# Performance work log

Hardware: AMD Instinct MI355X
Metric: run time of the kernel (lower is better)

## Reference

```python
import jax, jax.numpy as jnp
import numpy as np

EMBED = 1024
B, S = 4, 2048


def setup_inputs() -> dict:
    key = jax.random.key(0)
    ks = jax.random.split(key, 10)
    scale = 1.0 / np.sqrt(EMBED)
    return {
        "query": jax.random.normal(ks[0], (B, S, EMBED), jnp.float32),
        "key": jax.random.normal(ks[1], (B, S, EMBED), jnp.float32),
        "value": jax.random.normal(ks[2], (B, S, EMBED), jnp.float32),
        "attn_mask": jnp.zeros((B, S, S), jnp.float32),
        "Wq": jax.random.normal(ks[3], (EMBED, EMBED), jnp.float32) * scale,
        "bq": jnp.zeros((EMBED,), jnp.float32),
        "Wk": jax.random.normal(ks[4], (EMBED, EMBED), jnp.float32) * scale,
        "bk": jnp.zeros((EMBED,), jnp.float32),
        "Wv": jax.random.normal(ks[5], (EMBED, EMBED), jnp.float32) * scale,
        "bv": jnp.zeros((EMBED,), jnp.float32),
    }


def reference(query, key, value, attn_mask, Wq, bq, Wk, bk, Wv, bv):
    # Linear projections (torch Linear: x @ W.T + b)
    q = jnp.einsum("bse,fe->bsf", query, Wq) + bq
    k = jnp.einsum("bse,fe->bsf", key, Wk) + bk
    v = jnp.einsum("bse,fe->bsf", value, Wv) + bv
    # Scaled dot-product attention; NOTE: scale is sqrt(embed_size) (full dim),
    # matching the original module exactly (num_heads is unused there).
    inv_scale = 1.0 / jnp.sqrt(jnp.asarray(q.shape[-1], q.dtype))
    qk = jnp.einsum("bqe,bke->bqk", q, k) * inv_scale + attn_mask
    attn = jax.nn.softmax(qk, axis=-1)
    # dropout_p = 0.0 (eval-mode identity)
    return jnp.einsum("bqk,bke->bqe", attn, v)
```

## Files before the change

kernel.cpp:

```cpp
#include <hip/hip_runtime.h>
#include <stdint.h>


typedef __attribute__((ext_vector_type(8))) short s8v;
typedef __attribute__((ext_vector_type(4))) float f32x4;
typedef __attribute__((ext_vector_type(4))) unsigned u32x4;

__device__ __forceinline__ unsigned short f2b(float f) {
  union { float f; unsigned u; } c; c.f = f;
  unsigned r = c.u + 0x7fffu + ((c.u >> 16) & 1u);
  return (unsigned short)(r >> 16);
}

__device__ __forceinline__ void gload_lds16(const void* gsrc, void* ldst) {
  __builtin_amdgcn_global_load_lds(
      (__attribute__((address_space(1))) unsigned int*)(uintptr_t)gsrc,
      (__attribute__((address_space(3))) unsigned int*)(unsigned)(uintptr_t)ldst,
      16, 0, 0);
}

template <int N> __device__ __forceinline__ void waitvm() {
  if constexpr (N == 4)      asm volatile("s_waitcnt vmcnt(4)" ::: "memory");
  else if constexpr (N == 3) asm volatile("s_waitcnt vmcnt(3)" ::: "memory");
  else                       asm volatile("s_waitcnt vmcnt(0)" ::: "memory");
}

struct JobF {
  const float* A; const float* B; unsigned short* C; const float* bias;
  long sAb, sBb, sCb;
  int lda, ldb, ldc, tilesN, tilesMN, bmode;
};

__global__ __launch_bounds__(512, 2) void gemmF(JobF j0, JobF j1, JobF j2,
                                                int b0, int b1) {
  constexpr int ASLOT = 256 * 64;
  constexpr int SLOT = ASLOT + 128 * 64;
  constexpr int NT = 32;
  __shared__ __align__(16) char lds[4 * SLOT];

  const int nwg = gridDim.x;
  const int hw = blockIdx.x;
  int g = (hw & 7) * (nwg >> 3) + (hw >> 3);
  const JobF J = (g < b0) ? j0 : (g < b1) ? j1 : j2;
  g -= (g < b0) ? 0 : (g < b1) ? b0 : b1;

  const int batch = g / J.tilesMN;
  const int tt = g - batch * J.tilesMN;
  const int tm = tt / J.tilesN, tn = tt - tm * J.tilesN;
  const int brow = tm << 8, bcol = tn << 7;

  const int tid = threadIdx.x, lane = tid & 63, w = tid >> 6;
  const int wm = w >> 2, wn = w & 3;
  const int fr = lane & 15, fq = lane >> 4;

  const float* Ab = J.A + (long)batch * J.sAb;
  const float* Bb = J.B + (long)batch * J.sBb;

  const float* gsrcF[3];
  int ldsdst[3];
#pragma unroll
  for (int i = 0; i < 3; i++) {
    const int c = w + i * 8;
    const bool isA = (c < 16);
    const int cc = isA ? c : c - 16;
    const int roff = cc * 1024 + lane * 16;
    const int L = roff ^ (((roff >> 7) & 7) << 4);
    const int row = L >> 6, elem = (L & 63) >> 1;
    gsrcF[i] = (isA ? (Ab + (long)(brow + row) * J.lda)
                    : (Bb + (long)(bcol + row) * J.ldb)) + elem;
    ldsdst[i] = (isA ? 0 : ASLOT) + cc * 1024 + lane * 16;
  }

  int offA[8], offB[2];
#pragma unroll
  for (int mi = 0; mi < 8; mi++) {
    const int oa = (wm * 128 + mi * 16 + fr) * 64 + fq * 16;
    offA[mi] = oa ^ (((oa >> 7) & 7) << 4);
  }
#pragma unroll
  for (int ni = 0; ni < 2; ni++) {
    const int ob = (wn * 32 + ni * 16 + fr) * 64 + fq * 16;
    offB[ni] = ASLOT + (ob ^ (((ob >> 7) & 7) << 4));
  }

  f32x4 acc[8][2];
#pragma unroll
  for (int mi = 0; mi < 8; mi++)
#pragma unroll
    for (int ni = 0; ni < 2; ni++) acc[mi][ni] = (f32x4){0.f, 0.f, 0.f, 0.f};

  f32x4 eLo[3], eHi[3], oLo[3], oHi[3];

#define ISSUE(kt, LO, HI) { \
  _Pragma("unroll") \
  for (int i_ = 0; i_ < 3; i_++) { \
    const float* p_ = gsrcF[i_] + (long)(kt) * 32; \
    LO[i_] = *(const f32x4*)p_; HI[i_] = *(const f32x4*)(p_ + 4); } }

#define CVTWRITE(kt, LO, HI) { \
  char* const sb_ = lds + ((kt) & 3) * SLOT; \
  _Pragma("unroll") \
  for (int i_ = 0; i_ < 3; i_++) { \
    unsigned o0_, o1_, o2_, o3_; \
    asm("v_cvt_pk_bf16_f32 %0, %1, %2" : "=v"(o0_) : "v"(LO[i_][0]), "v"(LO[i_][1])); \
    asm("v_cvt_pk_bf16_f32 %0, %1, %2" : "=v"(o1_) : "v"(LO[i_][2]), "v"(LO[i_][3])); \
    asm("v_cvt_pk_bf16_f32 %0, %1, %2" : "=v"(o2_) : "v"(HI[i_][0]), "v"(HI[i_][1])); \
    asm("v_cvt_pk_bf16_f32 %0, %1, %2" : "=v"(o3_) : "v"(HI[i_][2]), "v"(HI[i_][3])); \
    *(u32x4*)(sb_ + ldsdst[i_]) = (u32x4){o0_, o1_, o2_, o3_}; } }

#define MFMA_BODY(t) { \
  const char* sb_ = lds + ((t) & 3) * SLOT; \
  s8v bf_[2], af_[4]; \
  _Pragma("unroll") \
  for (int ni_ = 0; ni_ < 2; ni_++) bf_[ni_] = *(const s8v*)(sb_ + offB[ni_]); \
  _Pragma("unroll") \
  for (int mi_ = 0; mi_ < 4; mi_++) af_[mi_] = *(const s8v*)(sb_ + offA[mi_]); \
  __builtin_amdgcn_s_setprio(1); \
  _Pragma("unroll") \
  for (int mi_ = 0; mi_ < 4; mi_++) \
    _Pragma("unroll") \
    for (int ni_ = 0; ni_ < 2; ni_++) \
      acc[mi_][ni_] = __builtin_amdgcn_mfma_f32_16x16x32_bf16( \
          af_[mi_], bf_[ni_], acc[mi_][ni_], 0, 0, 0); \
  __builtin_amdgcn_s_setprio(0); \
  _Pragma("unroll") \
  for (int mi_ = 0; mi_ < 4; mi_++) af_[mi_] = *(const s8v*)(sb_ + offA[4 + mi_]); \
  __builtin_amdgcn_s_setprio(1); \
  _Pragma("unroll") \
  for (int mi_ = 0; mi_ < 4; mi_++) \
    _Pragma("unroll") \
    for (int ni_ = 0; ni_ < 2; ni_++) \
      acc[4 + mi_][ni_] = __builtin_amdgcn_mfma_f32_16x16x32_bf16( \
          af_[mi_], bf_[ni_], acc[4 + mi_][ni_], 0, 0, 0); \
  __builtin_amdgcn_s_setprio(0); }

#define ENDBAR() { \
  asm volatile("s_waitcnt lgkmcnt(0)" ::: "memory"); \
  __builtin_amdgcn_s_barrier(); }

  ISSUE(0, eLo, eHi);
  ISSUE(1, oLo, oHi);
  CVTWRITE(0, eLo, eHi);
  ENDBAR();
  ISSUE(2, eLo, eHi);

  for (int t = 0; t < NT; t += 2) {
    MFMA_BODY(t);
    if (t + 1 < NT) {
      CVTWRITE(t + 1, oLo, oHi);
      if (t + 3 < NT) ISSUE(t + 3, oLo, oHi);
      ENDBAR();
      MFMA_BODY(t + 1);
      if (t + 2 < NT) {
        CVTWRITE(t + 2, eLo, eHi);
        if (t + 4 < NT) ISSUE(t + 4, eLo, eHi);
        ENDBAR();
      }
    }
  }

  const long cB = (long)batch * J.sCb;
#pragma unroll
  for (int mi = 0; mi < 8; mi++) {
    const int rbase = brow + wm * 128 + mi * 16 + fq * 4;
#pragma unroll
    for (int ni = 0; ni < 2; ni++) {
      const int col = bcol + wn * 32 + ni * 16 + fr;
      const float bc = (J.bmode == 1) ? J.bias[col] : 0.f;
#pragma unroll
      for (int r = 0; r < 4; r++) {
        const int row = rbase + r;
        float v = acc[mi][ni][r] + ((J.bmode == 2) ? J.bias[row] : bc);
        J.C[cB + (long)row * J.ldc + col] = f2b(v);
      }
    }
  }
#undef ISSUE
#undef CVTWRITE
#undef MFMA_BODY
#undef ENDBAR
}

struct Job {
  const unsigned short* A; const unsigned short* B; void* C;
  const float* bias; const float* mask; float* sRow;
  long sAb, sBb, sCb, sMb;
  int lda, ldb, ldc, ldM;
  int K, tilesN, tilesMN;
  float scale; int bmode;
};

template <int NFRAG, int MODE>
__global__ __launch_bounds__(512, 2) void gemmJ(Job j0, Job j1, Job j2,
                                                int b0, int b1) {
  constexpr int BN = NFRAG * 64;
  constexpr int ASLOT = 256 * 64;
  constexpr int BSLOT = BN * 64;
  constexpr int SLOT = ASLOT + BSLOT;
  constexpr int CH = SLOT / 1024;
  constexpr int GPW = CH / 8;
  static_assert(4 * SLOT <= 160 * 1024, "LDS budget");
  __shared__ __align__(16) char lds[4 * SLOT];

  const int nwg = gridDim.x;
  const int hw = blockIdx.x;
  int g = (hw & 7) * (nwg >> 3) + (hw >> 3);
  const Job J = (g < b0) ? j0 : (g < b1) ? j1 : j2;
  g -= (g < b0) ? 0 : (g < b1) ? b0 : b1;

  const int batch = g / J.tilesMN;
  const int tt = g - batch * J.tilesMN;
  const int tm = tt / J.tilesN, tn = tt - tm * J.tilesN;
  const int brow = tm << 8, bcol = tn * BN;

  const int tid = threadIdx.x;
  const int lane = tid & 63, w = tid >> 6;
  const int wm = w >> 2, wn = w & 3;
  const int fr = lane & 15, fq = lane >> 4;

  const unsigned short* Ab = J.A + (long)batch * J.sAb;
  const unsigned short* Bb = J.B + (long)batch * J.sBb;

  const unsigned short* gsrc[GPW];
  int ldsdst[GPW];
#pragma unroll
  for (int i = 0; i < GPW; i++) {
    const int c = w + i * 8;
    const bool isA = (c < 16);
    const int cc = isA ? c : c - 16;
    const int roff = cc * 1024 + lane * 16;
    const int L = roff ^ (((roff >> 7) & 7) << 4);
    const int row = L >> 6, colb = L & 63;
    gsrc[i] = (isA ? (Ab + (long)(brow + row) * J.lda)
                   : (Bb + (long)(bcol + row) * J.ldb)) + (colb >> 1);
    ldsdst[i] = (isA ? 0 : ASLOT) + cc * 1024;
  }

  int offA[8], offB[NFRAG];
#pragma unroll
  for (int mi = 0; mi < 8; mi++) {
    const int oa = (wm * 128 + mi * 16 + fr) * 64 + fq * 16;
    offA[mi] = oa ^ (((oa >> 7) & 7) << 4);
  }
#pragma unroll
  for (int ni = 0; ni < NFRAG; ni++) {
    const int ob = (wn * (NFRAG * 16) + ni * 16 + fr) * 64 + fq * 16;
    offB[ni] = ASLOT + (ob ^ (((ob >> 7) & 7) << 4));
  }

  f32x4 acc[8][NFRAG];
#pragma unroll
  for (int mi = 0; mi < 8; mi++)
#pragma unroll
    for (int ni = 0; ni < NFRAG; ni++) acc[mi][ni] = (f32x4){0.f, 0.f, 0.f, 0.f};

  const int NT = J.K >> 5;

#define STAGE(kt) { \
  char* const sb_ = lds + ((kt) & 3) * SLOT; \
  _Pragma("unroll") \
  for (int i_ = 0; i_ < GPW; i_++) \
    gload_lds16(gsrc[i_] + (long)(kt) * 32, sb_ + ldsdst[i_]); }

  STAGE(0);
  STAGE(1);
  waitvm<GPW>();
  __builtin_amdgcn_s_barrier();

  for (int t = 0; t < NT; ++t) {
    const char* sb = lds + (t & 3) * SLOT;
    if (t + 2 < NT) STAGE(t + 2);

    s8v bf[NFRAG], af[4];
#pragma unroll
    for (int ni = 0; ni < NFRAG; ni++) bf[ni] = *(const s8v*)(sb + offB[ni]);
#pragma unroll
    for (int mi = 0; mi < 4; mi++) af[mi] = *(const s8v*)(sb + offA[mi]);
    __builtin_amdgcn_s_setprio(1);
#pragma unroll
    for (int mi = 0; mi < 4; mi++)
#pragma unroll
      for (int ni = 0; ni < NFRAG; ni++)
        acc[mi][ni] = __builtin_amdgcn_mfma_f32_16x16x32_bf16(
            af[mi], bf[ni], acc[mi][ni], 0, 0, 0);
    __builtin_amdgcn_s_setprio(0);
#pragma unroll
    for (int mi = 0; mi < 4; mi++) af[mi] = *(const s8v*)(sb + offA[4 + mi]);
    __builtin_amdgcn_s_setprio(1);
#pragma unroll
    for (int mi = 0; mi < 4; mi++)
#pragma unroll
      for (int ni = 0; ni < NFRAG; ni++)
        acc[4 + mi][ni] = __builtin_amdgcn_mfma_f32_16x16x32_bf16(
            af[mi], bf[ni], acc[4 + mi][ni], 0, 0, 0);
    __builtin_amdgcn_s_setprio(0);

    if (t + 1 < NT) {
      if (t + 2 < NT) waitvm<GPW>();
      else            waitvm<0>();
      __builtin_amdgcn_s_barrier();
    }
  }

  unsigned short* Cb = (unsigned short*)J.C;
  float* Cf = (float*)J.C;
  const long cB = (long)batch * J.sCb;
  const float* maskB = (MODE == 1) ? (J.mask + (long)batch * J.sMb) : nullptr;
  float* sB = (J.sRow != nullptr) ? (J.sRow + batch * 2048) : nullptr;

#pragma unroll
  for (int mi = 0; mi < 8; mi++) {
    const int rbase = brow + wm * 128 + mi * 16 + fq * 4;

    if constexpr (MODE == 1) {
      float rs[4] = {0.f, 0.f, 0.f, 0.f};
#pragma unroll
      for (int ni = 0; ni < NFRAG; ni++) {
        const int col = bcol + wn * (NFRAG * 16) + ni * 16 + fr;
#pragma unroll
        for (int r = 0; r < 4; r++) {
          const int row = rbase + r;
          float v = acc[mi][ni][r] * J.scale + maskB[(long)row * J.ldM + col];
          v = __expf(v);
          Cb[cB + (long)row * J.ldc + col] = f2b(v);
          rs[r] += v;
        }
      }
#pragma unroll
      for (int off = 1; off < 16; off <<= 1) {
#pragma unroll
        for (int r = 0; r < 4; r++) rs[r] += __shfl_xor(rs[r], off, 64);
      }
      if (fr == 0) {
#pragma unroll
        for (int r = 0; r < 4; r++) atomicAdd(&sB[rbase + r], rs[r]);
      }
    } else {
      float inv[4];
#pragma unroll
      for (int r = 0; r < 4; r++) inv[r] = 1.0f / sB[rbase + r];
#pragma unroll
      for (int ni = 0; ni < NFRAG; ni++) {
        const int col = bcol + wn * (NFRAG * 16) + ni * 16 + fr;
#pragma unroll
        for (int r = 0; r < 4; r++) {
          const int row = rbase + r;
          Cf[cB + (long)row * J.ldc + col] = acc[mi][ni][r] * inv[r];
        }
      }
    }
  }
#undef STAGE
}

__global__ __launch_bounds__(256) void zeroS(float* sz) {
  sz[blockIdx.x * 256 + threadIdx.x] = 0.f;
}

extern "C" void kernel_launch(void* const* d_in, const int* in_sizes, int n_in,
                              void* d_out, int out_size, void* d_ws, size_t ws_size,
                              hipStream_t stream) {
  const float* q    = (const float*)d_in[0];
  const float* k    = (const float*)d_in[1];
  const float* v    = (const float*)d_in[2];
  const float* mask = (const float*)d_in[3];
  const float* Wq   = (const float*)d_in[4];
  const float* bq   = (const float*)d_in[5];
  const float* Wk   = (const float*)d_in[6];
  const float* bk   = (const float*)d_in[7];
  const float* Wv   = (const float*)d_in[8];
  const float* bv   = (const float*)d_in[9];
  float* out = (float*)d_out;

  const size_t MB = 1ull << 20;
  if (ws_size < 134 * MB) return;
  char* ws = (char*)d_ws;
  unsigned short* qb  = (unsigned short*)(ws + 0 * MB);
  unsigned short* kb  = (unsigned short*)(ws + 16 * MB);
  unsigned short* vT  = (unsigned short*)(ws + 32 * MB);
  float*          sRw = (float*)(ws + 48 * MB);
  unsigned short* Sb  = (unsigned short*)(ws + 80 * MB);

  zeroS<<<32, 256, 0, stream>>>(sRw);

  JobF fq = { q, Wq, qb, bq, 0, 0, 0, 1024, 1024, 1024, 8, 256, 1 };
  JobF fk = { k, Wk, kb, bk, 0, 0, 0, 1024, 1024, 1024, 8, 256, 1 };
  JobF fv = { Wv, v, vT, bv, 0, 2048L * 1024, 1024L * 2048,
              1024, 1024, 2048, 16, 64, 2 };
  gemmF<<<768, 512, 0, stream>>>(fq, fk, fv, 256, 512);

  Job js = { qb, kb, (void*)Sb, nullptr, mask, sRw,
             2048L * 1024, 2048L * 1024, 2048L * 2048, 2048L * 2048,
             1024, 1024, 2048, 2048, 1024, 8, 64, 0.03125f, 0 };
  gemmJ<4, 1><<<256, 512, 0, stream>>>(js, js, js, 256, 256);

  Job jp = { Sb, vT, (void*)out, nullptr, nullptr, sRw,
             2048L * 2048, 1024L * 2048, 2048L * 1024, 0,
             2048, 2048, 1024, 0, 2048, 8, 64, 1.0f, 0 };
  gemmJ<2, 2><<<256, 512, 0, stream>>>(jp, jp, jp, 256, 256);
}
```

Measured before the change: 221.6 us.

## Double K-tile depth in fp32-input projection GEMM with triple-buffered LDS

```diff
diff --git a/kernel.cpp b/kernel.cpp
--- a/kernel.cpp
+++ b/kernel.cpp
@@ -31,12 +31,12 @@
   int lda, ldb, ldc, tilesN, tilesMN, bmode;
 };
 
-__global__ __launch_bounds__(512, 2) void gemmF(JobF j0, JobF j1, JobF j2,
+__global__ __launch_bounds__(512, 1) void gemmF(JobF j0, JobF j1, JobF j2,
                                                 int b0, int b1) {
-  constexpr int ASLOT = 256 * 64;
-  constexpr int SLOT = ASLOT + 128 * 64;
-  constexpr int NT = 32;
-  __shared__ __align__(16) char lds[4 * SLOT];
+  constexpr int ASLOT = 256 * 128;
+  constexpr int SLOT = ASLOT + 128 * 128;
+  constexpr int NT = 16;
+  __shared__ __align__(16) char lds[3 * SLOT];
 
   const int nwg = gridDim.x;
   const int hw = blockIdx.x;
@@ -56,16 +56,16 @@
   const float* Ab = J.A + (long)batch * J.sAb;
   const float* Bb = J.B + (long)batch * J.sBb;
 
-  const float* gsrcF[3];
-  int ldsdst[3];
-#pragma unroll
-  for (int i = 0; i < 3; i++) {
+  const float* gsrcF[6];
+  int ldsdst[6];
+#pragma unroll
+  for (int i = 0; i < 6; i++) {
     const int c = w + i * 8;
-    const bool isA = (c < 16);
-    const int cc = isA ? c : c - 16;
+    const bool isA = (c < 32);
+    const int cc = isA ? c : c - 32;
     const int roff = cc * 1024 + lane * 16;
     const int L = roff ^ (((roff >> 7) & 7) << 4);
-    const int row = L >> 6, elem = (L & 63) >> 1;
+    const int row = L >> 7, elem = (L & 127) >> 1;
     gsrcF[i] = (isA ? (Ab + (long)(brow + row) * J.lda)
                     : (Bb + (long)(bcol + row) * J.ldb)) + elem;
     ldsdst[i] = (isA ? 0 : ASLOT) + cc * 1024 + lane * 16;
@@ -74,13 +74,13 @@
   int offA[8], offB[2];
 #pragma unroll
   for (int mi = 0; mi < 8; mi++) {
-    const int oa = (wm * 128 + mi * 16 + fr) * 64 + fq * 16;
-    offA[mi] = oa ^ (((oa >> 7) & 7) << 4);
+    const int rA = wm * 128 + mi * 16 + fr;
+    offA[mi] = rA * 128 + ((fq * 16) ^ ((rA & 7) << 4));
   }
 #pragma unroll
   for (int ni = 0; ni < 2; ni++) {
-    const int ob = (wn * 32 + ni * 16 + fr) * 64 + fq * 16;
-    offB[ni] = ASLOT + (ob ^ (((ob >> 7) & 7) << 4));
+    const int rB = wn * 32 + ni * 16 + fr;
+    offB[ni] = ASLOT + rB * 128 + ((fq * 16) ^ ((rB & 7) << 4));
   }
 
   f32x4 acc[8][2];
@@ -89,74 +89,70 @@
 #pragma unroll
     for (int ni = 0; ni < 2; ni++) acc[mi][ni] = (f32x4){0.f, 0.f, 0.f, 0.f};
 
-  f32x4 eLo[3], eHi[3], oLo[3], oHi[3];
-
-#define ISSUE(kt, LO, HI) { \
-  _Pragma("unroll") \
-  for (int i_ = 0; i_ < 3; i_++) { \
-    const float* p_ = gsrcF[i_] + (long)(kt) * 32; \
-    LO[i_] = *(const f32x4*)p_; HI[i_] = *(const f32x4*)(p_ + 4); } }
-
-#define CVTWRITE(kt, LO, HI) { \
-  char* const sb_ = lds + ((kt) & 3) * SLOT; \
-  _Pragma("unroll") \
-  for (int i_ = 0; i_ < 3; i_++) { \
+  f32x4 sLo[6], sHi[6];
+
+#define ISSUE(kt) { \
+  _Pragma("unroll") \
+  for (int i_ = 0; i_ < 6; i_++) { \
+    const float* p_ = gsrcF[i_] + (long)(kt) * 64; \
+    sLo[i_] = *(const f32x4*)p_; sHi[i_] = *(const f32x4*)(p_ + 4); } }
+
+#define CVTWRITE(sb_) { \
+  _Pragma("unroll") \
+  for (int i_ = 0; i_ < 6; i_++) { \
     unsigned o0_, o1_, o2_, o3_; \
-    asm("v_cvt_pk_bf16_f32 %0, %1, %2" : "=v"(o0_) : "v"(LO[i_][0]), "v"(LO[i_][1])); \
-    asm("v_cvt_pk_bf16_f32 %0, %1, %2" : "=v"(o1_) : "v"(LO[i_][2]), "v"(LO[i_][3])); \
-    asm("v_cvt_pk_bf16_f32 %0, %1, %2" : "=v"(o2_) : "v"(HI[i_][0]), "v"(HI[i_][1])); \
-    asm("v_cvt_pk_bf16_f32 %0, %1, %2" : "=v"(o3_) : "v"(HI[i_][2]), "v"(HI[i_][3])); \
-    *(u32x4*)(sb_ + ldsdst[i_]) = (u32x4){o0_, o1_, o2_, o3_}; } }
-
-#define MFMA_BODY(t) { \
-  const char* sb_ = lds + ((t) & 3) * SLOT; \
-  s8v bf_[2], af_[4]; \
-  _Pragma("unroll") \
-  for (int ni_ = 0; ni_ < 2; ni_++) bf_[ni_] = *(const s8v*)(sb_ + offB[ni_]); \
-  _Pragma("unroll") \
-  for (int mi_ = 0; mi_ < 4; mi_++) af_[mi_] = *(const s8v*)(sb_ + offA[mi_]); \
+    asm("v_cvt_pk_bf16_f32 %0, %1, %2" : "=v"(o0_) : "v"(sLo[i_][0]), "v"(sLo[i_][1])); \
+    asm("v_cvt_pk_bf16_f32 %0, %1, %2" : "=v"(o1_) : "v"(sLo[i_][2]), "v"(sLo[i_][3])); \
+    asm("v_cvt_pk_bf16_f32 %0, %1, %2" : "=v"(o2_) : "v"(sHi[i_][0]), "v"(sHi[i_][1])); \
+    asm("v_cvt_pk_bf16_f32 %0, %1, %2" : "=v"(o3_) : "v"(sHi[i_][2]), "v"(sHi[i_][3])); \
+    *(u32x4*)((sb_) + ldsdst[i_]) = (u32x4){o0_, o1_, o2_, o3_}; } }
+
+#define MFMA_HALF(sb_, AM) { \
+  s8v af_[4][2]; \
+  _Pragma("unroll") \
+  for (int mi_ = 0; mi_ < 4; mi_++) { \
+    af_[mi_][0] = *(const s8v*)((sb_) + offA[(AM) + mi_]); \
+    af_[mi_][1] = *(const s8v*)((sb_) + (offA[(AM) + mi_] ^ 64)); } \
   __builtin_amdgcn_s_setprio(1); \
   _Pragma("unroll") \
-  for (int mi_ = 0; mi_ < 4; mi_++) \
+  for (int ks_ = 0; ks_ < 2; ks_++) \
     _Pragma("unroll") \
-    for (int ni_ = 0; ni_ < 2; ni_++) \
-      acc[mi_][ni_] = __builtin_amdgcn_mfma_f32_16x16x32_bf16( \
-          af_[mi_], bf_[ni_], acc[mi_][ni_], 0, 0, 0); \
-  __builtin_amdgcn_s_setprio(0); \
-  _Pragma("unroll") \
-  for (int mi_ = 0; mi_ < 4; mi_++) af_[mi_] = *(const s8v*)(sb_ + offA[4 + mi_]); \
-  __builtin_amdgcn_s_setprio(1); \
-  _Pragma("unroll") \
-  for (int mi_ = 0; mi_ < 4; mi_++) \
-    _Pragma("unroll") \
-    for (int ni_ = 0; ni_ < 2; ni_++) \
-      acc[4 + mi_][ni_] = __builtin_amdgcn_mfma_f32_16x16x32_bf16( \
-          af_[mi_], bf_[ni_], acc[4 + mi_][ni_], 0, 0, 0); \
+    for (int mi_ = 0; mi_ < 4; mi_++) \
+      _Pragma("unroll") \
+      for (int ni_ = 0; ni_ < 2; ni_++) \
+        acc[(AM) + mi_][ni_] = __builtin_amdgcn_mfma_f32_16x16x32_bf16( \
+            af_[mi_][ks_], bf_[ni_][ks_], acc[(AM) + mi_][ni_], 0, 0, 0); \
   __builtin_amdgcn_s_setprio(0); }
+
+#define MFMA_BODY(sb_) { \
+  s8v bf_[2][2]; \
+  _Pragma("unroll") \
+  for (int ni_ = 0; ni_ < 2; ni_++) { \
+    bf_[ni_][0] = *(const s8v*)((sb_) + offB[ni_]); \
+    bf_[ni_][1] = *(const s8v*)((sb_) + (offB[ni_] ^ 64)); } \
+  MFMA_HALF(sb_, 0); \
+  MFMA_HALF(sb_, 4); }
 
 #define ENDBAR() { \
   asm volatile("s_waitcnt lgkmcnt(0)" ::: "memory"); \
   __builtin_amdgcn_s_barrier(); }
 
-  ISSUE(0, eLo, eHi);
-  ISSUE(1, oLo, oHi);
-  CVTWRITE(0, eLo, eHi);
+  ISSUE(0);
+  CVTWRITE(lds);
+  ISSUE(1);
   ENDBAR();
-  ISSUE(2, eLo, eHi);
-
-  for (int t = 0; t < NT; t += 2) {
-    MFMA_BODY(t);
+
+  int sCur = 0;
+  for (int t = 0; t < NT; ++t) {
+    const char* sb = lds + sCur * SLOT;
+    int sNxt = sCur + 1; if (sNxt == 3) sNxt = 0;
+    MFMA_BODY(sb);
     if (t + 1 < NT) {
-      CVTWRITE(t + 1, oLo, oHi);
-      if (t + 3 < NT) ISSUE(t + 3, oLo, oHi);
+      CVTWRITE(lds + sNxt * SLOT);
+      if (t + 2 < NT) ISSUE(t + 2);
       ENDBAR();
-      MFMA_BODY(t + 1);
-      if (t + 2 < NT) {
-        CVTWRITE(t + 2, eLo, eHi);
-        if (t + 4 < NT) ISSUE(t + 4, eLo, eHi);
-        ENDBAR();
-      }
     }
+    sCur = sNxt;
   }
 
   const long cB = (long)batch * J.sCb;
@@ -177,6 +173,7 @@
   }
 #undef ISSUE
 #undef CVTWRITE
+#undef MFMA_HALF
 #undef MFMA_BODY
 #undef ENDBAR
 }
```

Measured after the change: 225.2 us. No clear change (+1.6%).
